# Kernel tuning notes

Measured on AMD Instinct MI355X. Metric: run time of the kernel, lower is better.

The kernel has to match this reference:

```python
import jax, jax.numpy as jnp
import numpy as np
from jax import lax

B, T, I, H, O = 64, 512, 256, 1024, 1


def setup_inputs() -> dict:
    key = jax.random.key(0)
    ks = jax.random.split(key, 7)
    s_ih = 1.0 / np.sqrt(H)
    return {
        "x": jax.random.normal(ks[0], (B, T, I), dtype=jnp.float32),
        "W_ih": jax.random.uniform(ks[1], (4 * H, I), minval=-s_ih, maxval=s_ih, dtype=jnp.float32),
        "W_hh": jax.random.uniform(ks[2], (4 * H, H), minval=-s_ih, maxval=s_ih, dtype=jnp.float32),
        "b_ih": jax.random.uniform(ks[3], (4 * H,), minval=-s_ih, maxval=s_ih, dtype=jnp.float32),
        "b_hh": jax.random.uniform(ks[4], (4 * H,), minval=-s_ih, maxval=s_ih, dtype=jnp.float32),
        "fc_W": jax.random.uniform(ks[5], (O, H), minval=-s_ih, maxval=s_ih, dtype=jnp.float32),
        "fc_b": jax.random.uniform(ks[6], (O,), minval=-s_ih, maxval=s_ih, dtype=jnp.float32),
    }


def reference(x, W_ih, W_hh, b_ih, b_hh, fc_W, fc_b):
    Bd, Td, _ = x.shape
    Hd = W_hh.shape[1]
    # Precompute input projections for all timesteps: [T, B, 4H]
    x_proj = jnp.einsum('bti,gi->tbg', x, W_ih) + b_ih + b_hh

    def step(carry, xt):
        h, c = carry
        gates = xt + h @ W_hh.T  # [B, 4H]
        i_g, f_g, g_g, o_g = jnp.split(gates, 4, axis=-1)  # PyTorch order i,f,g,o
        i_g = jax.nn.sigmoid(i_g)
        f_g = jax.nn.sigmoid(f_g)
        g_g = jnp.tanh(g_g)
        o_g = jax.nn.sigmoid(o_g)
        c_new = f_g * c + i_g * g_g
        h_new = o_g * jnp.tanh(c_new)
        return (h_new, c_new), None

    h0 = jnp.zeros((Bd, Hd), dtype=x.dtype)
    c0 = jnp.zeros((Bd, Hd), dtype=x.dtype)
    (h_last, _), _ = lax.scan(step, (h0, c0), x_proj)
    out = jnp.tanh(h_last)          # tanh on last hidden state
    return out @ fc_W.T + fc_b      # [B, O]
```

## Files before the change

kernel.cpp:

```cpp
#include <hip/hip_runtime.h>
#include <hip/hip_bf16.h>


typedef __bf16 bf16_t;
typedef bf16_t b16x8 __attribute__((ext_vector_type(8)));
typedef float  f32x4 __attribute__((ext_vector_type(4)));

#define TQ 512
#define IQ 256
#define HQ 1024

#define RED(w,g,u,b) (((((w)*4 + (g))*16 + (u))*20) + (b))

#define HCOPY 131072
#define HPBUF 65536
#define BCOPY 4096

union U8 { b16x8 b; unsigned long long q[2]; unsigned short u[8]; };
union HU { f32x4 f; b16x8 b; };

__device__ __forceinline__ float bf2f(unsigned short s) {
    return __uint_as_float(((unsigned)s) << 16);
}
__device__ __forceinline__ unsigned short f2bf(float f) {
    unsigned u = __float_as_uint(f);
    u += 0x7fff + ((u >> 16) & 1);
    return (unsigned short)(u >> 16);
}
__device__ __forceinline__ b16x8 cvt84(float4 a, float4 b) {
    U8 r;
    r.u[0] = f2bf(a.x); r.u[1] = f2bf(a.y); r.u[2] = f2bf(a.z); r.u[3] = f2bf(a.w);
    r.u[4] = f2bf(b.x); r.u[5] = f2bf(b.y); r.u[6] = f2bf(b.z); r.u[7] = f2bf(b.w);
    return r.b;
}
__device__ __forceinline__ float frcp(float x) { return __builtin_amdgcn_rcpf(x); }
__device__ __forceinline__ float sigm(float x) {
    return frcp(1.f + __expf(-x));
}
__device__ __forceinline__ float tanh_f(float v) {
    float x = fminf(fmaxf(v, -15.f), 15.f);
    float e = __expf(2.f * x);
    return (e - 1.f) * frcp(e + 1.f);
}

__device__ __forceinline__ void load_h64_sys(b16x8* ah, const unsigned short* p0) {
    HU h0, h1, h2, h3;
    asm volatile(
        "global_load_dwordx4 %0, %4, off sc0 sc1\n\t"
        "global_load_dwordx4 %1, %4, off offset:64 sc0 sc1\n\t"
        "global_load_dwordx4 %2, %4, off offset:128 sc0 sc1\n\t"
        "global_load_dwordx4 %3, %4, off offset:192 sc0 sc1\n\t"
        "s_waitcnt vmcnt(0)"
        : "=&v"(h0.f), "=&v"(h1.f), "=&v"(h2.f), "=&v"(h3.f)
        : "v"(p0)
        : "memory");
    ah[0] = h0.b; ah[1] = h1.b; ah[2] = h2.b; ah[3] = h3.b;
}

__launch_bounds__(512, 2)
__global__ void lstm_persist(const float* __restrict__ x,
                             const float* __restrict__ Wih,
                             const float* __restrict__ Whh,
                             const float* __restrict__ bih,
                             const float* __restrict__ bhh,
                             const float* __restrict__ fcW,
                             const float* __restrict__ fcb,
                             float* __restrict__ out,
                             unsigned short* __restrict__ hbuf,
                             unsigned int* __restrict__ bar)
{
    __shared__ float red[8 * 4 * 16 * 20];

    const int tid  = threadIdx.x;
    const int w    = tid >> 6;
    const int lane = tid & 63;
    const int bid  = blockIdx.x;
    const int bg   = bid & 3;
    const int ug   = bid >> 2;
    const int par  = ug & 1;

    const int l16  = lane & 15;
    const int quad = lane >> 4;

    b16x8 wih[4];
    b16x8 whh[4][4];
    {
        const int koff = quad * 8;
        #pragma unroll
        for (int g = 0; g < 4; ++g) {
            int row = g * HQ + ug * 16 + l16;
            const float* p = Wih + (size_t)row * IQ + w * 32 + koff;
            float4 a = *(const float4*)p;
            float4 b = *(const float4*)(p + 4);
            wih[g] = cvt84(a, b);
            #pragma unroll
            for (int j = 0; j < 4; ++j) {
                int k0 = (w * 4 + j) * 32 + koff;
                const float* q = Whh + (size_t)row * HQ + k0;
                float4 c = *(const float4*)q;
                float4 e = *(const float4*)(q + 4);
                whh[j][g] = cvt84(c, e);
            }
        }
    }

    const int hi  = (lane >> 5) & 1;
    const int eb  = 2 * w + hi;
    const int dup = (lane >> 4) & 1;
    float c_st = 0.f;
    float bias_g[4];
    #pragma unroll
    for (int g = 0; g < 4; ++g) {
        int gr = g * HQ + ug * 16 + l16;
        bias_g[g] = bih[gr] + bhh[gr];
    }

    const unsigned short* hrd0 = hbuf + (size_t)par * HCOPY
                               + ((size_t)bg * 16 + l16) * HQ + w * 128 + quad * 8;
    unsigned short* hwr0 = hbuf + (size_t)bg * 16 * HQ + (size_t)eb * HQ + ug * 16 + l16;

    const unsigned int* myfl = bar + (size_t)par * BCOPY
                             + ((size_t)(bg * 64 + w * 8 + (lane >> 3)) * 16 + (lane & 7));
    unsigned int* wfl0 = bar + ((size_t)(bg * 64 + ug) * 16 + w);
    unsigned int* wfl1 = wfl0 + BCOPY;

    const float* xbase = x + ((size_t)(bg * 16 + l16) * TQ) * IQ + w * 32 + quad * 8;
    float4 xa = *(const float4*)(xbase);
    float4 xb = *(const float4*)(xbase + 4);

    for (int t = 0; t < TQ; ++t) {
        const int p = t & 1;

        b16x8 ax = cvt84(xa, xb);
        f32x4 acc[4];
        #pragma unroll
        for (int g = 0; g < 4; ++g) {
            f32x4 z = {0.f, 0.f, 0.f, 0.f};
            acc[g] = __builtin_amdgcn_mfma_f32_16x16x32_bf16(ax, wih[g], z, 0, 0, 0);
        }

        const unsigned need = (unsigned)t;
        {
            unsigned v = __hip_atomic_load(myfl, __ATOMIC_RELAXED,
                                           __HIP_MEMORY_SCOPE_AGENT);
            while (!__all(v >= need))
                v = __hip_atomic_load(myfl, __ATOMIC_RELAXED,
                                      __HIP_MEMORY_SCOPE_AGENT);
        }

        b16x8 ah[4];
        load_h64_sys(ah, hrd0 + (size_t)p * HPBUF);
        #pragma unroll
        for (int j = 0; j < 4; ++j) {
            #pragma unroll
            for (int g = 0; g < 4; ++g)
                acc[g] = __builtin_amdgcn_mfma_f32_16x16x32_bf16(ah[j], whh[j][g], acc[g], 0, 0, 0);
        }

        __syncthreads();

        #pragma unroll
        for (int g = 0; g < 4; ++g)
            *(f32x4*)&red[RED(w, g, l16, quad * 4)] = acc[g];
        __syncthreads();

        float s[4];
        #pragma unroll
        for (int g = 0; g < 4; ++g) {
            float a0 = red[RED(dup * 4 + 0, g, l16, eb)]
                     + red[RED(dup * 4 + 1, g, l16, eb)];
            float a1 = red[RED(dup * 4 + 2, g, l16, eb)]
                     + red[RED(dup * 4 + 3, g, l16, eb)];
            float as = a0 + a1;
            as += __shfl_xor(as, 16);
            s[g] = as;
        }
        {
            float gi = s[0] + bias_g[0];
            float gf = s[1] + bias_g[1];
            float gg = s[2] + bias_g[2];
            float go = s[3] + bias_g[3];
            float i_s = sigm(gi);
            float f_s = sigm(gf);
            float g_t = tanh_f(gg);
            float o_s = sigm(go);
            float c = f_s * c_st + i_s * g_t;
            c_st = c;
            float h = o_s * tanh_f(c);
            if (!dup) {
                unsigned short hv = f2bf(h);
                __hip_atomic_store(hwr0 + (size_t)(p ^ 1) * HPBUF, hv,
                                   __ATOMIC_RELAXED, __HIP_MEMORY_SCOPE_AGENT);
                __hip_atomic_store(hwr0 + HCOPY + (size_t)(p ^ 1) * HPBUF, hv,
                                   __ATOMIC_RELAXED, __HIP_MEMORY_SCOPE_AGENT);
            }
        }
        asm volatile("s_waitcnt vmcnt(0)" ::: "memory");
        if (lane == 0) {
            __hip_atomic_store(wfl0, (unsigned)(t + 1),
                               __ATOMIC_RELAXED, __HIP_MEMORY_SCOPE_AGENT);
            __hip_atomic_store(wfl1, (unsigned)(t + 1),
                               __ATOMIC_RELAXED, __HIP_MEMORY_SCOPE_AGENT);
        }

        size_t nt = (t + 1 < TQ) ? (size_t)(t + 1) * IQ : (size_t)t * IQ;
        xa = *(const float4*)(xbase + nt);
        xb = *(const float4*)(xbase + nt + 4);
    }

    if (bid < 4) {
        #pragma unroll
        for (int pb = 0; pb < 8; ++pb) {
            const unsigned int* pf = bar + ((size_t)(bg * 64 + pb * 8 + (lane >> 3)) * 16 + (lane & 7));
            unsigned v = __hip_atomic_load(pf, __ATOMIC_RELAXED,
                                           __HIP_MEMORY_SCOPE_AGENT);
            while (!__all(v >= (unsigned)TQ))
                v = __hip_atomic_load(pf, __ATOMIC_RELAXED,
                                      __HIP_MEMORY_SCOPE_AGENT);
        }
        const unsigned short* hl = hbuf + (size_t)bg * 16 * HQ;
        float fb = fcb[0];
        #pragma unroll
        for (int r = 0; r < 2; ++r) {
            int b = w * 2 + r;
            float sacc = 0.f;
            #pragma unroll
            for (int j = 0; j < 16; ++j) {
                int u = j * 64 + lane;
                unsigned short hv = __hip_atomic_load(hl + (size_t)b * HQ + u,
                                                      __ATOMIC_RELAXED,
                                                      __HIP_MEMORY_SCOPE_AGENT);
                sacc += tanh_f(bf2f(hv)) * fcW[u];
            }
            #pragma unroll
            for (int off = 32; off > 0; off >>= 1)
                sacc += __shfl_down(sacc, off);
            if (lane == 0) out[bg * 16 + b] = sacc + fb;
        }
    }
}

extern "C" void kernel_launch(void* const* d_in, const int* in_sizes, int n_in,
                              void* d_out, int out_size, void* d_ws, size_t ws_size,
                              hipStream_t stream) {
    (void)in_sizes; (void)n_in; (void)out_size; (void)ws_size;
    const float* x   = (const float*)d_in[0];
    const float* Wih = (const float*)d_in[1];
    const float* Whh = (const float*)d_in[2];
    const float* bih = (const float*)d_in[3];
    const float* bhh = (const float*)d_in[4];
    const float* fcW = (const float*)d_in[5];
    const float* fcb = (const float*)d_in[6];
    float* out = (float*)d_out;

    unsigned short* hbuf = (unsigned short*)d_ws;
    unsigned int*   bar  = (unsigned int*)((char*)d_ws + 524288);

    hipMemsetAsync(d_ws, 0, 524288 + 32768, stream);

    void* args[] = { &x, &Wih, &Whh, &bih, &bhh, &fcW, &fcb, &out, &hbuf, &bar };
    hipLaunchCooperativeKernel(reinterpret_cast<void*>(lstm_persist),
                               dim3(256), dim3(512), args, 0, stream);
}
```

Before: 2.100 ms.

## Add 512-block LSTM persistent kernel with 8-batch groups and fallback

Adds a new persistent cooperative kernel that splits the batch into 8 groups of 8 rows across 512 blocks of 256 threads. Each wave now holds twice as much of W_hh and W_ih in registers, and the reduction over k spans 4 waves instead of 8. The first step skips the recurrent matmul because h starts at zero. The final FC is gathered through a separate h buffer guarded by its own flag barrier. The host checks occupancy and falls back to the old kernel if two blocks per CU are not possible. The aim is to spread the sequential recurrence across more blocks so each step has less per-block work, at the cost of more cross-block flag traffic and higher register pressure.

```diff
diff --git a/kernel.cpp b/kernel.cpp
--- a/kernel.cpp
+++ b/kernel.cpp
@@ -5,16 +5,11 @@
 typedef __bf16 bf16_t;
 typedef bf16_t b16x8 __attribute__((ext_vector_type(8)));
 typedef float  f32x4 __attribute__((ext_vector_type(4)));
+typedef unsigned u32x4 __attribute__((ext_vector_type(4)));
 
 #define TQ 512
 #define IQ 256
 #define HQ 1024
-
-#define RED(w,g,u,b) (((((w)*4 + (g))*16 + (u))*20) + (b))
-
-#define HCOPY 131072
-#define HPBUF 65536
-#define BCOPY 4096
 
 union U8 { b16x8 b; unsigned long long q[2]; unsigned short u[8]; };
 union HU { f32x4 f; b16x8 b; };
@@ -34,40 +29,268 @@
     return r.b;
 }
 __device__ __forceinline__ float frcp(float x) { return __builtin_amdgcn_rcpf(x); }
-__device__ __forceinline__ float sigm(float x) {
-    return frcp(1.f + __expf(-x));
-}
+__device__ __forceinline__ float sigm(float x) { return frcp(1.f + __expf(-x)); }
 __device__ __forceinline__ float tanh_f(float v) {
     float x = fminf(fmaxf(v, -15.f), 15.f);
     float e = __expf(2.f * x);
     return (e - 1.f) * frcp(e + 1.f);
 }
 
-__device__ __forceinline__ void load_h64_sys(b16x8* ah, const unsigned short* p0) {
-    HU h0, h1, h2, h3;
+__device__ __forceinline__ unsigned ld_flag_sys(const unsigned* p) {
+    unsigned v;
+    asm volatile("global_load_dword %0, %1, off sc0 sc1\n\ts_waitcnt vmcnt(0)"
+                 : "=v"(v) : "v"(p) : "memory");
+    return v;
+}
+__device__ __forceinline__ void st_flag_sys(unsigned* p, unsigned v) {
+    asm volatile("global_store_dword %0, %1, off sc0 sc1" :: "v"(p), "v"(v) : "memory");
+}
+__device__ __forceinline__ void st_h16_sys(unsigned short* p, unsigned short v) {
+    asm volatile("global_store_short %0, %1, off sc0 sc1" :: "v"(p), "v"(v) : "memory");
+}
+__device__ __forceinline__ void ld_h4(b16x8* ah, const unsigned short* p) {
+    HU a, b, c, d;
     asm volatile(
         "global_load_dwordx4 %0, %4, off sc0 sc1\n\t"
         "global_load_dwordx4 %1, %4, off offset:64 sc0 sc1\n\t"
         "global_load_dwordx4 %2, %4, off offset:128 sc0 sc1\n\t"
         "global_load_dwordx4 %3, %4, off offset:192 sc0 sc1\n\t"
         "s_waitcnt vmcnt(0)"
-        : "=&v"(h0.f), "=&v"(h1.f), "=&v"(h2.f), "=&v"(h3.f)
-        : "v"(p0)
-        : "memory");
-    ah[0] = h0.b; ah[1] = h1.b; ah[2] = h2.b; ah[3] = h3.b;
-}
+        : "=&v"(a.f), "=&v"(b.f), "=&v"(c.f), "=&v"(d.f) : "v"(p) : "memory");
+    ah[0] = a.b; ah[1] = b.b; ah[2] = c.b; ah[3] = d.b;
+}
+__device__ __forceinline__ void ld_h2_dev(b16x8* ah, const unsigned short* p) {
+    HU a, b;
+    asm volatile(
+        "global_load_dwordx4 %0, %2, off sc0 sc1\n\t"
+        "global_load_dwordx4 %1, %2, off offset:16 sc0 sc1\n\t"
+        "s_waitcnt vmcnt(0)"
+        : "=&v"(a.f), "=&v"(b.f) : "v"(p) : "memory");
+    ah[0] = a.b; ah[1] = b.b;
+}
+__device__ __forceinline__ u32x4 ld_flag4_dev(const unsigned* p) {
+    u32x4 v;
+    asm volatile("global_load_dwordx4 %0, %1, off sc0 sc1\n\ts_waitcnt vmcnt(0)"
+                 : "=v"(v) : "v"(p) : "memory");
+    return v;
+}
+
+#define A_HCOPY_SH 131072
+#define A_HBG_SH   16384
+#define A_HPBUF_SH 8192
+#define A_BCOPY_W  8192
+#define A_OFF_FH    524288
+#define A_OFF_BAR   655360
+#define A_OFF_FBAR  720896
+#define MEMSET_BYTES 753664
+#define RED2(ww,g,u,b) (((((ww)*4 + (g))*16 + (u))*12) + (b))
+
+__launch_bounds__(256, 2)
+__global__ void lstm_a(const float* __restrict__ x,
+                       const float* __restrict__ Wih,
+                       const float* __restrict__ Whh,
+                       const float* __restrict__ bih,
+                       const float* __restrict__ bhh,
+                       const float* __restrict__ fcW,
+                       const float* __restrict__ fcb,
+                       float* __restrict__ out,
+                       char* __restrict__ ws)
+{
+    __shared__ float red[4 * 4 * 16 * 12];
+
+    unsigned short* hb   = (unsigned short*)ws;
+    unsigned short* fh   = (unsigned short*)(ws + A_OFF_FH);
+    unsigned*       bar  = (unsigned*)(ws + A_OFF_BAR);
+    unsigned*       fbar = (unsigned*)(ws + A_OFF_FBAR);
+
+    const int tid  = threadIdx.x;
+    const int w    = tid >> 6;
+    const int lane = tid & 63;
+    const int bid  = blockIdx.x;
+    const int bg   = bid & 7;
+    const int ug   = bid >> 3;
+    const int par  = ug & 1;
+
+    const int l16  = lane & 15;
+    const int quad = lane >> 4;
+
+    b16x8 wih[2][4];
+    b16x8 whh[8][4];
+    {
+        const int koff = quad * 8;
+        #pragma unroll
+        for (int g = 0; g < 4; ++g) {
+            int row = g * HQ + ug * 16 + l16;
+            #pragma unroll
+            for (int c = 0; c < 2; ++c) {
+                const float* p = Wih + (size_t)row * IQ + w * 64 + c * 32 + koff;
+                wih[c][g] = cvt84(*(const float4*)p, *(const float4*)(p + 4));
+            }
+            #pragma unroll
+            for (int j = 0; j < 8; ++j) {
+                const float* q = Whh + (size_t)row * HQ + w * 256 + j * 32 + koff;
+                whh[j][g] = cvt84(*(const float4*)q, *(const float4*)(q + 4));
+            }
+        }
+    }
+
+    const int hi  = (lane >> 5) & 1;
+    const int eb  = 2 * w + hi;
+    const int dup = (lane >> 4) & 1;
+    float c_st = 0.f, h_last = 0.f;
+    float bias_g[4];
+    #pragma unroll
+    for (int g = 0; g < 4; ++g) {
+        int gr = g * HQ + ug * 16 + l16;
+        bias_g[g] = bih[gr] + bhh[gr];
+    }
+
+    const unsigned short* hrd0 = hb + (size_t)par * A_HCOPY_SH + (size_t)bg * A_HBG_SH
+                               + (size_t)(l16 & 7) * 1024 + w * 256 + quad * 8;
+    unsigned short* hwr0 = hb + (size_t)bg * A_HBG_SH + (size_t)eb * 1024 + ug * 16 + l16;
+    const unsigned* myfl = bar + (size_t)par * A_BCOPY_W
+                         + ((size_t)(bg * 64 + w * 16 + (lane >> 2)) * 16 + (lane & 3));
+    unsigned* wfl0 = bar + ((size_t)(bg * 64 + ug) * 16 + w);
+    unsigned* wfl1 = wfl0 + A_BCOPY_W;
+
+    const float* xbase = x + ((size_t)(bg * 8 + (l16 & 7)) * TQ) * IQ + w * 64 + quad * 8;
+    float4 xa = *(const float4*)(xbase);
+    float4 xb = *(const float4*)(xbase + 4);
+    float4 xc = *(const float4*)(xbase + 32);
+    float4 xd = *(const float4*)(xbase + 36);
+
+    for (int t = 0; t < TQ; ++t) {
+        const int p = t & 1;
+
+        b16x8 ax0 = cvt84(xa, xb);
+        b16x8 ax1 = cvt84(xc, xd);
+        f32x4 acc[4];
+        #pragma unroll
+        for (int g = 0; g < 4; ++g) {
+            f32x4 z = {0.f, 0.f, 0.f, 0.f};
+            acc[g] = __builtin_amdgcn_mfma_f32_16x16x32_bf16(ax0, wih[0][g], z, 0, 0, 0);
+            acc[g] = __builtin_amdgcn_mfma_f32_16x16x32_bf16(ax1, wih[1][g], acc[g], 0, 0, 0);
+        }
+
+        if (t) {
+            const unsigned need = (unsigned)t;
+            unsigned v = ld_flag_sys(myfl);
+            while (!__all(v >= need)) v = ld_flag_sys(myfl);
+
+            const unsigned short* hp = hrd0 + (size_t)p * A_HPBUF_SH;
+            b16x8 ah[4];
+            ld_h4(ah, hp);
+            #pragma unroll
+            for (int j = 0; j < 4; ++j) {
+                #pragma unroll
+                for (int g = 0; g < 4; ++g)
+                    acc[g] = __builtin_amdgcn_mfma_f32_16x16x32_bf16(ah[j], whh[j][g], acc[g], 0, 0, 0);
+            }
+            ld_h4(ah, hp + 128);
+            #pragma unroll
+            for (int j = 0; j < 4; ++j) {
+                #pragma unroll
+                for (int g = 0; g < 4; ++g)
+                    acc[g] = __builtin_amdgcn_mfma_f32_16x16x32_bf16(ah[j], whh[4 + j][g], acc[g], 0, 0, 0);
+            }
+        }
+
+        __syncthreads();
+        if (quad < 2) {
+            #pragma unroll
+            for (int g = 0; g < 4; ++g)
+                *(f32x4*)&red[RED2(w, g, l16, quad * 4)] = acc[g];
+        }
+        __syncthreads();
+
+        float s[4];
+        #pragma unroll
+        for (int g = 0; g < 4; ++g) {
+            float a0 = red[RED2(dup * 2 + 0, g, l16, eb)]
+                     + red[RED2(dup * 2 + 1, g, l16, eb)];
+            s[g] = a0 + __shfl_xor(a0, 16);
+        }
+        {
+            float gi = s[0] + bias_g[0];
+            float gf = s[1] + bias_g[1];
+            float gg = s[2] + bias_g[2];
+            float go_ = s[3] + bias_g[3];
+            float i_s = sigm(gi);
+            float f_s = sigm(gf);
+            float g_t = tanh_f(gg);
+            float o_s = sigm(go_);
+            float c = f_s * c_st + i_s * g_t;
+            c_st = c;
+            float h = o_s * tanh_f(c);
+            h_last = h;
+            if (!dup) {
+                unsigned short hv = f2bf(h);
+                st_h16_sys(hwr0 + (size_t)(p ^ 1) * A_HPBUF_SH, hv);
+                st_h16_sys(hwr0 + A_HCOPY_SH + (size_t)(p ^ 1) * A_HPBUF_SH, hv);
+            }
+        }
+        asm volatile("s_waitcnt vmcnt(0)" ::: "memory");
+        if (lane == 0) {
+            st_flag_sys(wfl0, (unsigned)(t + 1));
+            st_flag_sys(wfl1, (unsigned)(t + 1));
+        }
+
+        size_t nt = (t + 1 < TQ) ? (size_t)(t + 1) * IQ : (size_t)t * IQ;
+        xa = *(const float4*)(xbase + nt);
+        xb = *(const float4*)(xbase + nt + 4);
+        xc = *(const float4*)(xbase + nt + 32);
+        xd = *(const float4*)(xbase + nt + 36);
+    }
+
+    if (!dup)
+        st_h16_sys(fh + ((size_t)(bg * 8 + eb)) * 1024 + ug * 16 + l16, f2bf(h_last));
+    asm volatile("s_waitcnt vmcnt(0)" ::: "memory");
+    if (lane == 0) st_flag_sys(fbar + ((size_t)(bg * 64 + ug) * 16 + w), 1u);
+
+    if (ug == 0) {
+        const unsigned* pf = fbar + ((size_t)(bg * 64 + lane) * 16);
+        for (;;) {
+            u32x4 v = ld_flag4_dev(pf);
+            if (__all(v[0] == 1u && v[1] == 1u && v[2] == 1u && v[3] == 1u)) break;
+        }
+        float fb = fcb[0];
+        #pragma unroll
+        for (int r = 0; r < 2; ++r) {
+            int b = w * 2 + r;
+            b16x8 hv[2];
+            ld_h2_dev(hv, fh + ((size_t)(bg * 8 + b)) * 1024 + lane * 16);
+            float sacc = 0.f;
+            #pragma unroll
+            for (int k = 0; k < 2; ++k) {
+                U8 u; u.b = hv[k];
+                #pragma unroll
+                for (int e = 0; e < 8; ++e)
+                    sacc += tanh_f(bf2f(u.u[e])) * fcW[lane * 16 + k * 8 + e];
+            }
+            #pragma unroll
+            for (int off = 32; off > 0; off >>= 1)
+                sacc += __shfl_down(sacc, off);
+            if (lane == 0) out[bg * 8 + b] = sacc + fb;
+        }
+    }
+}
+
+#define RED_B(w,g,u,b) (((((w)*4 + (g))*16 + (u))*20) + (b))
+#define B_HCOPY 131072
+#define B_HPBUF 65536
+#define B_BCOPY 4096
 
 __launch_bounds__(512, 2)
-__global__ void lstm_persist(const float* __restrict__ x,
-                             const float* __restrict__ Wih,
-                             const float* __restrict__ Whh,
-                             const float* __restrict__ bih,
-                             const float* __restrict__ bhh,
-                             const float* __restrict__ fcW,
-                             const float* __restrict__ fcb,
-                             float* __restrict__ out,
-                             unsigned short* __restrict__ hbuf,
-                             unsigned int* __restrict__ bar)
+__global__ void lstm_b(const float* __restrict__ x,
+                       const float* __restrict__ Wih,
+                       const float* __restrict__ Whh,
+                       const float* __restrict__ bih,
+                       const float* __restrict__ bhh,
+                       const float* __restrict__ fcW,
+                       const float* __restrict__ fcb,
+                       float* __restrict__ out,
+                       unsigned short* __restrict__ hbuf,
+                       unsigned int* __restrict__ bar)
 {
     __shared__ float red[8 * 4 * 16 * 20];
 
@@ -115,14 +338,14 @@
         bias_g[g] = bih[gr] + bhh[gr];
     }
 
-    const unsigned short* hrd0 = hbuf + (size_t)par * HCOPY
+    const unsigned short* hrd0 = hbuf + (size_t)par * B_HCOPY
                                + ((size_t)bg * 16 + l16) * HQ + w * 128 + quad * 8;
     unsigned short* hwr0 = hbuf + (size_t)bg * 16 * HQ + (size_t)eb * HQ + ug * 16 + l16;
 
-    const unsigned int* myfl = bar + (size_t)par * BCOPY
+    const unsigned int* myfl = bar + (size_t)par * B_BCOPY
                              + ((size_t)(bg * 64 + w * 8 + (lane >> 3)) * 16 + (lane & 7));
     unsigned int* wfl0 = bar + ((size_t)(bg * 64 + ug) * 16 + w);
-    unsigned int* wfl1 = wfl0 + BCOPY;
+    unsigned int* wfl1 = wfl0 + B_BCOPY;
 
     const float* xbase = x + ((size_t)(bg * 16 + l16) * TQ) * IQ + w * 32 + quad * 8;
     float4 xa = *(const float4*)(xbase);
@@ -149,7 +372,7 @@
         }
 
         b16x8 ah[4];
-        load_h64_sys(ah, hrd0 + (size_t)p * HPBUF);
+        ld_h4(ah, hrd0 + (size_t)p * B_HPBUF);
         #pragma unroll
         for (int j = 0; j < 4; ++j) {
             #pragma unroll
@@ -158,19 +381,18 @@
         }
 
         __syncthreads();
-
         #pragma unroll
         for (int g = 0; g < 4; ++g)
-            *(f32x4*)&red[RED(w, g, l16, quad * 4)] = acc[g];
+            *(f32x4*)&red[RED_B(w, g, l16, quad * 4)] = acc[g];
         __syncthreads();
 
         float s[4];
         #pragma unroll
         for (int g = 0; g < 4; ++g) {
-            float a0 = red[RED(dup * 4 + 0, g, l16, eb)]
-                     + red[RED(dup * 4 + 1, g, l16, eb)];
-            float a1 = red[RED(dup * 4 + 2, g, l16, eb)]
-                     + red[RED(dup * 4 + 3, g, l16, eb)];
+            float a0 = red[RED_B(dup * 4 + 0, g, l16, eb)]
+                     + red[RED_B(dup * 4 + 1, g, l16, eb)];
+            float a1 = red[RED_B(dup * 4 + 2, g, l16, eb)]
+                     + red[RED_B(dup * 4 + 3, g, l16, eb)];
             float as = a0 + a1;
             as += __shfl_xor(as, 16);
             s[g] = as;
@@ -179,19 +401,19 @@
             float gi = s[0] + bias_g[0];
             float gf = s[1] + bias_g[1];
             float gg = s[2] + bias_g[2];
-            float go = s[3] + bias_g[3];
+            float go_ = s[3] + bias_g[3];
             float i_s = sigm(gi);
             float f_s = sigm(gf);
             float g_t = tanh_f(gg);
-            float o_s = sigm(go);
+            float o_s = sigm(go_);
             float c = f_s * c_st + i_s * g_t;
             c_st = c;
             float h = o_s * tanh_f(c);
             if (!dup) {
                 unsigned short hv = f2bf(h);
-                __hip_atomic_store(hwr0 + (size_t)(p ^ 1) * HPBUF, hv,
+                __hip_atomic_store(hwr0 + (size_t)(p ^ 1) * B_HPBUF, hv,
                                    __ATOMIC_RELAXED, __HIP_MEMORY_SCOPE_AGENT);
-                __hip_atomic_store(hwr0 + HCOPY + (size_t)(p ^ 1) * HPBUF, hv,
+                __hip_atomic_store(hwr0 + B_HCOPY + (size_t)(p ^ 1) * B_HPBUF, hv,
                                    __ATOMIC_RELAXED, __HIP_MEMORY_SCOPE_AGENT);
             }
         }
@@ -253,12 +475,28 @@
     const float* fcb = (const float*)d_in[6];
     float* out = (float*)d_out;
 
+    hipMemsetAsync(d_ws, 0, MEMSET_BYTES, stream);
+
+    static int mode = -1;
+    if (mode < 0) {
+        int nb = 0;
+        hipError_t e = hipOccupancyMaxActiveBlocksPerMultiprocessor(
+            &nb, reinterpret_cast<const void*>(lstm_a), 256, 0);
+        mode = (e == hipSuccess && nb >= 2) ? 1 : 0;
+    }
+
+    if (mode == 1) {
+        char* ws = (char*)d_ws;
+        void* args[] = { &x, &Wih, &Whh, &bih, &bhh, &fcW, &fcb, &out, &ws };
+        hipError_t e = hipLaunchCooperativeKernel(
+            reinterpret_cast<void*>(lstm_a), dim3(512), dim3(256), args, 0, stream);
+        if (e == hipSuccess) return;
+        mode = 0;
+    }
+
     unsigned short* hbuf = (unsigned short*)d_ws;
     unsigned int*   bar  = (unsigned int*)((char*)d_ws + 524288);
-
-    hipMemsetAsync(d_ws, 0, 524288 + 32768, stream);
-
-    void* args[] = { &x, &Wih, &Whh, &bih, &bhh, &fcW, &fcb, &out, &hbuf, &bar };
-    hipLaunchCooperativeKernel(reinterpret_cast<void*>(lstm_persist),
-                               dim3(256), dim3(512), args, 0, stream);
-}
+    void* argsb[] = { &x, &Wih, &Whh, &bih, &bhh, &fcW, &fcb, &out, &hbuf, &bar };
+    hipLaunchCooperativeKernel(reinterpret_cast<void*>(lstm_b),
+                               dim3(256), dim3(512), argsb, 0, stream);
+}
```

After: 2.136 ms. No clear change (+1.7%).
